# Kernel tuning notes

Hardware: AMD Instinct MI355X
Metric: run time of the kernel (lower is better)

The kernel has to match this reference:

```python
import jax, jax.numpy as jnp
import numpy as np

B, S, E, DQ, DV = 8, 2048, 1024, 128, 128


def setup_inputs() -> dict:
    k0 = jax.random.key(0)
    ks = jax.random.split(k0, 10)
    scale_in = 1.0 / np.sqrt(E)
    return {
        "pad_mask": jax.random.uniform(ks[0], (B, S)) < 0.1,  # True = padded key position
        "query": jax.random.normal(ks[1], (B, S, E), jnp.float32),
        "key": jax.random.normal(ks[2], (B, S, E), jnp.float32),
        "value": jax.random.normal(ks[3], (B, S, E), jnp.float32),
        "Wq": jax.random.uniform(ks[4], (E, DQ), jnp.float32, -scale_in, scale_in),
        "bq": jnp.zeros((DQ,), jnp.float32),
        "Wk": jax.random.uniform(ks[5], (E, DQ), jnp.float32, -scale_in, scale_in),
        "bk": jnp.zeros((DQ,), jnp.float32),
        "Wv": jax.random.uniform(ks[6], (E, DV), jnp.float32, -scale_in, scale_in),
        "bv": jnp.zeros((DV,), jnp.float32),
    }


def reference(pad_mask, query, key, value, Wq, bq, Wk, bk, Wv, bv):
    # Linear projections (torch Linear: x @ W^T + b; weights stored pre-transposed here)
    q = query @ Wq + bq  # [B,S,DQ]
    k = key @ Wk + bk    # [B,S,DQ]
    v = value @ Wv + bv  # [B,S,DV]

    scores = jnp.einsum("bqd,bkd->bqk", q, k)  # [B,S,S]
    # Causal mask applied BEFORE scaling (as in source); -inf/scale is still -inf
    seq = scores.shape[1]
    causal = jnp.triu(jnp.ones((seq, seq), bool), k=1)
    scores = jnp.where(causal[None], -jnp.inf, scores)
    scores = scores / jnp.asarray(q.shape[-1] ** 0.5, scores.dtype)
    # Padding mask: mask key positions with -1e9 (broadcast over query dim)
    scores = jnp.where(pad_mask[:, None, :], jnp.asarray(-1e9, scores.dtype), scores)

    attn = jax.nn.softmax(scores, axis=-1)
    return jnp.einsum("bqk,bkd->bqd", attn, v)  # [B,S,DV]
```

## Files before the change

### kernel.cpp

```cpp
#include <hip/hip_runtime.h>
#include <hip/hip_bf16.h>

#define SEQ 2048
#define EMB 1024
#define DH  128
#define QSCALE 0.08838834764831845f

typedef __attribute__((ext_vector_type(4))) float f32x4;
typedef __attribute__((ext_vector_type(8))) short bf16x8;
typedef __attribute__((ext_vector_type(4))) short bf16x4;

__device__ __forceinline__ short f2bf(float f) {
  unsigned u = __builtin_bit_cast(unsigned, f);
  u += 0x7fffu + ((u >> 16) & 1u);
  return (short)(u >> 16);
}

__device__ __forceinline__ float bf2f(short s) {
  unsigned u = ((unsigned)(unsigned short)s) << 16;
  return __builtin_bit_cast(float, u);
}

__device__ __forceinline__ f32x4 mfma16(bf16x8 a, bf16x8 b, f32x4 c) {
  return __builtin_amdgcn_mfma_f32_16x16x32_bf16(a, b, c, 0, 0, 0);
}

__device__ __forceinline__ void gl_lds16(void* lds_base, const void* gsrc) {
  __builtin_amdgcn_global_load_lds(
      (const __attribute__((address_space(1))) void*)gsrc,
      (__attribute__((address_space(3))) void*)lds_base, 16, 0, 0);
}

__global__ void prep_weights(const float* __restrict__ Wq, const float* __restrict__ Wk,
                             const float* __restrict__ Wv, short* __restrict__ wt) {
  int p = blockIdx.x >> 7;
  int n = blockIdx.x & 127;
  const float* W = (p == 0) ? Wq : ((p == 1) ? Wk : Wv);
  int k0 = threadIdx.x * 4;
  bf16x4 v;
#pragma unroll
  for (int j = 0; j < 4; ++j) v[j] = f2bf(W[(k0 + j) * DH + n]);
  *(bf16x4*)(&wt[((p * DH + n) << 10) + k0]) = v;
}

__device__ __forceinline__ void proj_stage(float* a_lds, short* w_lds,
                                           const char* Xb, const char* Wb,
                                           int row0, int kk, int w, int lane) {
#pragma unroll
  for (int i = 0; i < 2; ++i) {
    int ch = w + i * 4;
    int phys = ch * 1024 + lane * 16;
    int lg = phys ^ (((phys >> 7) & 7) << 4);
    gl_lds16((char*)a_lds + ch * 1024,
             Xb + (size_t)(row0 + (lg >> 7)) * 4096 + kk * 128 + (lg & 127));
  }
#pragma unroll
  for (int i = 0; i < 2; ++i) {
    int ch = w + i * 4;
    int phys = ch * 1024 + lane * 16;
    int n = phys >> 6;
    int s = ((n ^ (n >> 2)) & 3) << 4;
    gl_lds16((char*)w_lds + ch * 1024,
             Wb + n * 2048 + kk * 64 + ((phys & 63) ^ s));
  }
}

__global__ __launch_bounds__(256) void proj_gemm(
    const float* __restrict__ Xq, const float* __restrict__ Xk, const float* __restrict__ Xv,
    const short* __restrict__ wt,
    const float* __restrict__ bq, const float* __restrict__ bk, const float* __restrict__ bv,
    short* __restrict__ qp, short* __restrict__ kp, short* __restrict__ vt) {
  __shared__ float a_lds[2][64 * 32];
  __shared__ short w_lds[2][128 * 32];
  const int tid = threadIdx.x;
  const int w = tid >> 6, lane = tid & 63;
  const int g = lane >> 4, c = lane & 15;
  const int p = blockIdx.x >> 8, mb = blockIdx.x & 255;
  const int row0 = mb << 6;
  const float* X    = (p == 0) ? Xq : ((p == 1) ? Xk : Xv);
  const float* bias = (p == 0) ? bq : ((p == 1) ? bk : bv);
  const char* Xb = (const char*)X;
  const char* Wb = (const char*)(wt + p * DH * EMB);

  f32x4 acc[8];
#pragma unroll
  for (int j = 0; j < 8; ++j) acc[j] = (f32x4){0.f, 0.f, 0.f, 0.f};

  const int arow = w * 16 + c;
  const int aswz = (arow & 7) << 4;
  const int ph_lo = (arow << 7) + ((g << 5) ^ aswz);

  proj_stage(a_lds[0], w_lds[0], Xb, Wb, row0, 0, w, lane);
  __syncthreads();

  for (int kk = 0; kk < 32; ++kk) {
    int cur = kk & 1;
    if (kk + 1 < 32)
      proj_stage(a_lds[cur ^ 1], w_lds[cur ^ 1], Xb, Wb, row0, kk + 1, w, lane);

    f32x4 lo = *(const f32x4*)((const char*)a_lds[cur] + ph_lo);
    f32x4 hi = *(const f32x4*)((const char*)a_lds[cur] + (ph_lo ^ 16));
    bf16x8 a;
#pragma unroll
    for (int j = 0; j < 4; ++j) { a[j] = f2bf(lo[j]); a[4 + j] = f2bf(hi[j]); }
#pragma unroll
    for (int nb = 0; nb < 8; ++nb) {
      int n = (nb << 4) + c;
      int s = ((n ^ (n >> 2)) & 3) << 4;
      bf16x8 b = *(const bf16x8*)((const char*)w_lds[cur] + (n << 6) + ((g << 4) ^ s));
      acc[nb] = mfma16(a, b, acc[nb]);
    }
    __syncthreads();
  }

  float bvals[8];
#pragma unroll
  for (int nb = 0; nb < 8; ++nb) bvals[nb] = bias[nb * 16 + c];

  if (p < 2) {
    short* outp = (p == 0) ? qp : kp;
    float sc = (p == 0) ? QSCALE : 1.0f;
#pragma unroll
    for (int r = 0; r < 4; ++r) {
      int token = row0 + w * 16 + g * 4 + r;
#pragma unroll
      for (int nb = 0; nb < 8; ++nb)
        outp[token * 128 + nb * 16 + c] = f2bf((acc[nb][r] + bvals[nb]) * sc);
    }
  } else {
    int tok0 = row0 + w * 16 + g * 4;
    int b_ = tok0 >> 11, s_ = tok0 & 2047;
#pragma unroll
    for (int nb = 0; nb < 8; ++nb) {
      int col = nb * 16 + c;
      bf16x4 v4;
#pragma unroll
      for (int r = 0; r < 4; ++r) v4[r] = f2bf(acc[nb][r] + bvals[nb]);
      *(bf16x4*)(&vt[((size_t)(b_ * 128 + col)) * 2048 + s_]) = v4;
    }
  }
}

__global__ __launch_bounds__(256) void avgv2_kernel(
    const short* __restrict__ vt, const int* __restrict__ pad,
    const float* __restrict__ bvv, float* __restrict__ avgv) {
  int b = blockIdx.x >> 3, dg = blockIdx.x & 7;
  int t = threadIdx.x, doff = t >> 4, sl = t & 15;
  int d = dg * 16 + doff;
  const short* vrow = vt + ((size_t)(b * 128 + d)) * 2048 + sl * 128;
  const int* prow = pad + (b << 11) + sl * 128;
  float sum = 0.f;
  int cnt = 0;
  for (int i = 0; i < 16; ++i) {
    bf16x8 v8 = *(const bf16x8*)(vrow + i * 8);
#pragma unroll
    for (int j = 0; j < 8; ++j) {
      int pd = prow[i * 8 + j];
      cnt += (pd != 0);
      if (pd) sum += bf2f(v8[j]);
    }
  }
#pragma unroll
  for (int xm = 1; xm < 16; xm <<= 1) {
    sum += __shfl_xor(sum, xm, 64);
    cnt += __shfl_xor(cnt, xm, 64);
  }
  if (sl == 0) avgv[(b << 7) + d] = (cnt > 0) ? (sum / (float)cnt) : 0.f;
  (void)bvv;
}

__device__ __forceinline__ void stage_kv(short* kb, short* vb,
                                         const char* kb_base, const char* vb_base,
                                         int kt, int w, int lane) {
#pragma unroll
  for (int ch = w; ch < 16; ch += 4) {
    int phys = ch * 1024 + lane * 16;
    int lg = phys ^ (((phys >> 8) & 7) << 4);
    gl_lds16((char*)kb + ch * 1024,
             kb_base + (size_t)(kt * 64 + (lg >> 8)) * 256 + (lg & 255));
  }
#pragma unroll
  for (int ch = w; ch < 16; ch += 4) {
    int phys = ch * 1024 + lane * 16;
    int lg = phys ^ (((phys >> 7) & 7) << 4);
    gl_lds16((char*)vb + ch * 1024,
             vb_base + (size_t)(lg >> 7) * 4096 + kt * 128 + (lg & 127));
  }
}

template <bool CAUSAL>
__device__ __forceinline__ void attn_tile(
    const short* __restrict__ k_lds, const short* __restrict__ v_lds, short* __restrict__ p_w,
    const bf16x8 (&qf)[4], f32x4 (&acc_o)[8], float (&m_r)[4], float (&l_r)[4],
    const int* __restrict__ padp, int kt, int qrow_g, int g, int c) {
  f32x4 sc[4];
#pragma unroll
  for (int nb = 0; nb < 4; ++nb) sc[nb] = (f32x4){0.f, 0.f, 0.f, 0.f};
#pragma unroll
  for (int ks = 0; ks < 4; ++ks) {
    bf16x8 kf[4];
#pragma unroll
    for (int nb = 0; nb < 4; ++nb) {
      int n = (nb << 4) + c;
      int off = (n << 8) + (ks << 6) + (g << 4);
      kf[nb] = *(const bf16x8*)((const char*)k_lds + (off ^ ((n & 7) << 4)));
    }
#pragma unroll
    for (int nb = 0; nb < 4; ++nb) sc[nb] = mfma16(qf[ks], kf[nb], sc[nb]);
  }

  int padv[4];
#pragma unroll
  for (int nb = 0; nb < 4; ++nb) padv[nb] = padp[kt + (nb << 4) + c];
  float sv[4][4];
#pragma unroll
  for (int nb = 0; nb < 4; ++nb) {
    bool pd = padv[nb] != 0;
    int key = kt + (nb << 4) + c;
#pragma unroll
    for (int r = 0; r < 4; ++r) {
      float s = sc[nb][r];
      if (CAUSAL && key > qrow_g + r) s = -1e30f;
      if (pd) s = -1e30f;
      sv[nb][r] = s;
    }
  }
  float tmax[4];
#pragma unroll
  for (int r = 0; r < 4; ++r)
    tmax[r] = fmaxf(fmaxf(sv[0][r], sv[1][r]), fmaxf(sv[2][r], sv[3][r]));
#pragma unroll
  for (int xm = 1; xm < 16; xm <<= 1)
#pragma unroll
    for (int r = 0; r < 4; ++r) tmax[r] = fmaxf(tmax[r], __shfl_xor(tmax[r], xm, 64));
  float al[4];
#pragma unroll
  for (int r = 0; r < 4; ++r) {
    float mn = fmaxf(m_r[r], tmax[r]);
    al[r] = __expf(m_r[r] - mn);
    m_r[r] = mn;
  }
  float ls[4] = {0.f, 0.f, 0.f, 0.f};
#pragma unroll
  for (int nb = 0; nb < 4; ++nb)
#pragma unroll
    for (int r = 0; r < 4; ++r) {
      float pp = __expf(sv[nb][r] - m_r[r]);
      sv[nb][r] = pp;
      ls[r] += pp;
    }
#pragma unroll
  for (int xm = 1; xm < 16; xm <<= 1)
#pragma unroll
    for (int r = 0; r < 4; ++r) ls[r] += __shfl_xor(ls[r], xm, 64);
#pragma unroll
  for (int r = 0; r < 4; ++r) l_r[r] = l_r[r] * al[r] + ls[r];
#pragma unroll
  for (int nb = 0; nb < 8; ++nb)
#pragma unroll
    for (int r = 0; r < 4; ++r) acc_o[nb][r] *= al[r];

#pragma unroll
  for (int nb = 0; nb < 4; ++nb)
#pragma unroll
    for (int r = 0; r < 4; ++r)
      p_w[(g * 4 + r) * 72 + (nb << 4) + c] = f2bf(sv[nb][r]);

#pragma unroll
  for (int ks = 0; ks < 2; ++ks) {
    bf16x8 pa = *(const bf16x8*)((const char*)p_w + c * 144 + ks * 64 + g * 16);
#pragma unroll
    for (int nb = 0; nb < 8; ++nb) {
      int n = (nb << 4) + c;
      int off = (n << 7) + (ks << 6) + (g << 4);
      bf16x8 vf = *(const bf16x8*)((const char*)v_lds + (off ^ ((n & 7) << 4)));
      acc_o[nb] = mfma16(pa, vf, acc_o[nb]);
    }
  }
}

__global__ __launch_bounds__(256) void flash_attn(
    const short* __restrict__ qp, const short* __restrict__ kp, const short* __restrict__ vt,
    const int* __restrict__ pad, float* __restrict__ partO, float* __restrict__ partML) {
  __shared__ short k_lds[2][64 * 128];
  __shared__ short v_lds[2][128 * 64];
  __shared__ short p_lds[4][16 * 72];
  const int tid = threadIdx.x, w = tid >> 6, lane = tid & 63;
  const int g = lane >> 4, c = lane & 15;
  const int j = blockIdx.x;
  int b, qi, half;
  if (j < 256) { b = j >> 5; qi = j & 31; half = 0; }
  else { int u = j - 256; b = u >> 5; qi = 31 - (u & 31); half = 1; }
  const int T = qi + 1;
  const int t0 = half ? (T >> 1) : 0;
  const int t1 = half ? T : (T >> 1);
  const int q0 = qi << 6;

  bf16x8 qf[4];
  {
    int token = (b << 11) + q0 + (w << 4) + c;
    const char* qrow = (const char*)qp + (size_t)token * 256;
#pragma unroll
    for (int s = 0; s < 4; ++s) qf[s] = *(const bf16x8*)(qrow + s * 64 + g * 16);
  }
  f32x4 acc_o[8];
#pragma unroll
  for (int i = 0; i < 8; ++i) acc_o[i] = (f32x4){0.f, 0.f, 0.f, 0.f};
  float m_r[4] = {-1e30f, -1e30f, -1e30f, -1e30f};
  float l_r[4] = {0.f, 0.f, 0.f, 0.f};

  const char* kb_base = (const char*)kp + (size_t)(b << 11) * 256;
  const char* vb_base = (const char*)vt + (size_t)b * 524288;
  const int* padp = pad + (b << 11);
  const int qrow_g = q0 + (w << 4) + (g << 2);

  if (t1 > t0) {
    stage_kv(k_lds[0], v_lds[0], kb_base, vb_base, t0, w, lane);
    __syncthreads();
    int cur = 0;
    for (int t = t0; t < t1; ++t) {
      if (t + 1 < t1)
        stage_kv(k_lds[cur ^ 1], v_lds[cur ^ 1], kb_base, vb_base, t + 1, w, lane);
      if (half && t == T - 1)
        attn_tile<true>(k_lds[cur], v_lds[cur], p_lds[w], qf, acc_o, m_r, l_r,
                        padp, t << 6, qrow_g, g, c);
      else
        attn_tile<false>(k_lds[cur], v_lds[cur], p_lds[w], qf, acc_o, m_r, l_r,
                         padp, t << 6, qrow_g, g, c);
      __syncthreads();
      cur ^= 1;
    }
  }

  float* pO = partO + (size_t)j * (64 * 128);
  float* pML = partML + (size_t)j * 128;
#pragma unroll
  for (int nb = 0; nb < 8; ++nb)
#pragma unroll
    for (int r = 0; r < 4; ++r)
      pO[(w * 16 + g * 4 + r) * 128 + (nb << 4) + c] = acc_o[nb][r];
  if (c == 0)
#pragma unroll
    for (int r = 0; r < 4; ++r) {
      pML[(w * 16 + g * 4 + r) * 2] = m_r[r];
      pML[(w * 16 + g * 4 + r) * 2 + 1] = l_r[r];
    }
}

__global__ __launch_bounds__(256) void combine_kernel(
    const float* __restrict__ partO, const float* __restrict__ partML,
    const float* __restrict__ avgv, float* __restrict__ out) {
  int gid = blockIdx.x * 256 + threadIdx.x;
  int row = gid >> 5;
  int d4 = gid & 31;
  int b = row >> 11, s = row & 2047;
  int qt = s >> 6, lr = s & 63;
  int wid1 = (b << 5) + qt;
  int wid2 = 256 + (b << 5) + (31 - qt);
  float m1 = partML[wid1 * 128 + lr * 2], l1 = partML[wid1 * 128 + lr * 2 + 1];
  float m2 = partML[wid2 * 128 + lr * 2], l2 = partML[wid2 * 128 + lr * 2 + 1];
  float m = fmaxf(m1, m2);
  f32x4 o;
  if (m < -1e8f) {
    o = *(const f32x4*)(avgv + (b << 7) + (d4 << 2));
  } else {
    float f1 = __expf(m1 - m), f2 = __expf(m2 - m);
    float inv = 1.0f / (l1 * f1 + l2 * f2);
    f32x4 o1 = *(const f32x4*)(partO + ((size_t)wid1 * 64 + lr) * 128 + (d4 << 2));
    f32x4 o2 = *(const f32x4*)(partO + ((size_t)wid2 * 64 + lr) * 128 + (d4 << 2));
#pragma unroll
    for (int k = 0; k < 4; ++k) o[k] = (o1[k] * f1 + o2[k] * f2) * inv;
  }
  *(f32x4*)(out + (size_t)row * 128 + (d4 << 2)) = o;
}

extern "C" void kernel_launch(void* const* d_in, const int* in_sizes, int n_in,
                              void* d_out, int out_size, void* d_ws, size_t ws_size,
                              hipStream_t stream) {
  const int*   pad   = (const int*)d_in[0];
  const float* query = (const float*)d_in[1];
  const float* key   = (const float*)d_in[2];
  const float* value = (const float*)d_in[3];
  const float* Wq    = (const float*)d_in[4];
  const float* bq    = (const float*)d_in[5];
  const float* Wk    = (const float*)d_in[6];
  const float* bk    = (const float*)d_in[7];
  const float* Wv    = (const float*)d_in[8];
  const float* bv    = (const float*)d_in[9];
  char* ws = (char*)d_ws;
  short* wt    = (short*)ws;
  short* qp    = (short*)(ws + 786432);
  short* kp    = (short*)(ws + 4980736);
  short* vt    = (short*)(ws + 9175040);
  float* partO = (float*)(ws + 13369344);
  float* partML= (float*)(ws + 30146560);
  float* avgv  = (float*)(ws + 30408704);
  float* out   = (float*)d_out;

  prep_weights<<<dim3(384), dim3(256), 0, stream>>>(Wq, Wk, Wv, wt);
  proj_gemm<<<dim3(768), dim3(256), 0, stream>>>(query, key, value, wt, bq, bk, bv, qp, kp, vt);
  avgv2_kernel<<<dim3(64), dim3(256), 0, stream>>>(vt, pad, bv, avgv);
  flash_attn<<<dim3(512), dim3(256), 0, stream>>>(qp, kp, vt, pad, partO, partML);
  combine_kernel<<<dim3(2048), dim3(256), 0, stream>>>(partO, partML, avgv, out);
}
```

Before: 97.21 us.

## Load projection operands directly to registers with MFMA-fragment weight layout

The projection GEMM drops its LDS double-buffered staging and instead has each wave load its A rows and pre-swizzled weight fragments straight from global memory into registers, using a two-stage register ping-pong for prefetch. prep_weights now writes the weights already laid out in MFMA B-fragment order, so each lane reads one contiguous 16-byte chunk. This removes LDS traffic and block-level barriers, but each of the four waves now reads the full weight tile separately and relies on cache for reuse. It also raises register pressure, with a launch bound hint of three blocks per CU.

Measured after the change: 120.2 us. 1.24x slower.

```diff
diff --git a/kernel.cpp b/kernel.cpp
--- a/kernel.cpp
+++ b/kernel.cpp
@@ -33,84 +33,76 @@
 
 __global__ void prep_weights(const float* __restrict__ Wq, const float* __restrict__ Wk,
                              const float* __restrict__ Wv, short* __restrict__ wt) {
-  int p = blockIdx.x >> 7;
-  int n = blockIdx.x & 127;
+  int gid = blockIdx.x * 256 + threadIdx.x;
+  int lane = gid & 63, c = lane & 15, g = (lane >> 4) & 3;
+  int nb = (gid >> 6) & 7;
+  int kk = (gid >> 9) & 31;
+  int p = gid >> 14;
   const float* W = (p == 0) ? Wq : ((p == 1) ? Wk : Wv);
-  int k0 = threadIdx.x * 4;
-  bf16x4 v;
-#pragma unroll
-  for (int j = 0; j < 4; ++j) v[j] = f2bf(W[(k0 + j) * DH + n]);
-  *(bf16x4*)(&wt[((p * DH + n) << 10) + k0]) = v;
-}
-
-__device__ __forceinline__ void proj_stage(float* a_lds, short* w_lds,
-                                           const char* Xb, const char* Wb,
-                                           int row0, int kk, int w, int lane) {
-#pragma unroll
-  for (int i = 0; i < 2; ++i) {
-    int ch = w + i * 4;
-    int phys = ch * 1024 + lane * 16;
-    int lg = phys ^ (((phys >> 7) & 7) << 4);
-    gl_lds16((char*)a_lds + ch * 1024,
-             Xb + (size_t)(row0 + (lg >> 7)) * 4096 + kk * 128 + (lg & 127));
-  }
-#pragma unroll
-  for (int i = 0; i < 2; ++i) {
-    int ch = w + i * 4;
-    int phys = ch * 1024 + lane * 16;
-    int n = phys >> 6;
-    int s = ((n ^ (n >> 2)) & 3) << 4;
-    gl_lds16((char*)w_lds + ch * 1024,
-             Wb + n * 2048 + kk * 64 + ((phys & 63) ^ s));
-  }
-}
-
-__global__ __launch_bounds__(256) void proj_gemm(
+  bf16x8 v;
+#pragma unroll
+  for (int j = 0; j < 8; ++j)
+    v[j] = f2bf(W[(kk * 32 + g * 8 + j) * DH + nb * 16 + c]);
+  *(bf16x8*)(&wt[(size_t)gid * 8]) = v;
+}
+
+__global__ __launch_bounds__(256, 3) void proj_gemm(
     const float* __restrict__ Xq, const float* __restrict__ Xk, const float* __restrict__ Xv,
     const short* __restrict__ wt,
     const float* __restrict__ bq, const float* __restrict__ bk, const float* __restrict__ bv,
     short* __restrict__ qp, short* __restrict__ kp, short* __restrict__ vt) {
-  __shared__ float a_lds[2][64 * 32];
-  __shared__ short w_lds[2][128 * 32];
   const int tid = threadIdx.x;
   const int w = tid >> 6, lane = tid & 63;
   const int g = lane >> 4, c = lane & 15;
   const int p = blockIdx.x >> 8, mb = blockIdx.x & 255;
-  const int row0 = mb << 6;
+  const int row0 = (mb << 6) + (w << 4);
   const float* X    = (p == 0) ? Xq : ((p == 1) ? Xk : Xv);
   const float* bias = (p == 0) ? bq : ((p == 1) ? bk : bv);
-  const char* Xb = (const char*)X;
-  const char* Wb = (const char*)(wt + p * DH * EMB);
+
+  const f32x4* ap = (const f32x4*)(X + (size_t)(row0 + c) * 1024 + (g << 3));
+  const bf16x8* wf = (const bf16x8*)(wt + ((size_t)p << 17)) + lane;
 
   f32x4 acc[8];
 #pragma unroll
-  for (int j = 0; j < 8; ++j) acc[j] = (f32x4){0.f, 0.f, 0.f, 0.f};
-
-  const int arow = w * 16 + c;
-  const int aswz = (arow & 7) << 4;
-  const int ph_lo = (arow << 7) + ((g << 5) ^ aswz);
-
-  proj_stage(a_lds[0], w_lds[0], Xb, Wb, row0, 0, w, lane);
-  __syncthreads();
-
-  for (int kk = 0; kk < 32; ++kk) {
-    int cur = kk & 1;
-    if (kk + 1 < 32)
-      proj_stage(a_lds[cur ^ 1], w_lds[cur ^ 1], Xb, Wb, row0, kk + 1, w, lane);
-
-    f32x4 lo = *(const f32x4*)((const char*)a_lds[cur] + ph_lo);
-    f32x4 hi = *(const f32x4*)((const char*)a_lds[cur] + (ph_lo ^ 16));
-    bf16x8 a;
-#pragma unroll
-    for (int j = 0; j < 4; ++j) { a[j] = f2bf(lo[j]); a[4 + j] = f2bf(hi[j]); }
-#pragma unroll
-    for (int nb = 0; nb < 8; ++nb) {
-      int n = (nb << 4) + c;
-      int s = ((n ^ (n >> 2)) & 3) << 4;
-      bf16x8 b = *(const bf16x8*)((const char*)w_lds[cur] + (n << 6) + ((g << 4) ^ s));
-      acc[nb] = mfma16(a, b, acc[nb]);
-    }
-    __syncthreads();
+  for (int i = 0; i < 8; ++i) acc[i] = (f32x4){0.f, 0.f, 0.f, 0.f};
+
+  f32x4 a0A, a1A, a0B, a1B;
+  bf16x8 bA[8], bB[8];
+
+  a0A = ap[0];
+  a1A = ap[1];
+#pragma unroll
+  for (int nb = 0; nb < 8; ++nb) bA[nb] = wf[nb << 6];
+
+#pragma unroll 1
+  for (int kk = 0; kk < 32; kk += 2) {
+    a0B = ap[(kk + 1) * 8];
+    a1B = ap[(kk + 1) * 8 + 1];
+#pragma unroll
+    for (int nb = 0; nb < 8; ++nb) bB[nb] = wf[(kk + 1) * 512 + (nb << 6)];
+
+    {
+      bf16x8 a;
+#pragma unroll
+      for (int j = 0; j < 4; ++j) { a[j] = f2bf(a0A[j]); a[4 + j] = f2bf(a1A[j]); }
+#pragma unroll
+      for (int nb = 0; nb < 8; ++nb) acc[nb] = mfma16(a, bA[nb], acc[nb]);
+    }
+
+    if (kk + 2 < 32) {
+      a0A = ap[(kk + 2) * 8];
+      a1A = ap[(kk + 2) * 8 + 1];
+#pragma unroll
+      for (int nb = 0; nb < 8; ++nb) bA[nb] = wf[(kk + 2) * 512 + (nb << 6)];
+    }
+
+    {
+      bf16x8 a;
+#pragma unroll
+      for (int j = 0; j < 4; ++j) { a[j] = f2bf(a0B[j]); a[4 + j] = f2bf(a1B[j]); }
+#pragma unroll
+      for (int nb = 0; nb < 8; ++nb) acc[nb] = mfma16(a, bB[nb], acc[nb]);
+    }
   }
 
   float bvals[8];
@@ -122,13 +114,13 @@
     float sc = (p == 0) ? QSCALE : 1.0f;
 #pragma unroll
     for (int r = 0; r < 4; ++r) {
-      int token = row0 + w * 16 + g * 4 + r;
+      int token = row0 + g * 4 + r;
 #pragma unroll
       for (int nb = 0; nb < 8; ++nb)
         outp[token * 128 + nb * 16 + c] = f2bf((acc[nb][r] + bvals[nb]) * sc);
     }
   } else {
-    int tok0 = row0 + w * 16 + g * 4;
+    int tok0 = row0 + g * 4;
     int b_ = tok0 >> 11, s_ = tok0 & 2047;
 #pragma unroll
     for (int nb = 0; nb < 8; ++nb) {
@@ -397,7 +389,7 @@
   float* avgv  = (float*)(ws + 30408704);
   float* out   = (float*)d_out;
 
-  prep_weights<<<dim3(384), dim3(256), 0, stream>>>(Wq, Wk, Wv, wt);
+  prep_weights<<<dim3(192), dim3(256), 0, stream>>>(Wq, Wk, Wv, wt);
   proj_gemm<<<dim3(768), dim3(256), 0, stream>>>(query, key, value, wt, bq, bk, bv, qp, kp, vt);
   avgv2_kernel<<<dim3(64), dim3(256), 0, stream>>>(vt, pad, bv, avgv);
   flash_attn<<<dim3(512), dim3(256), 0, stream>>>(qp, kp, vt, pad, partO, partML);
```
